# Kernel optimization log

Measured on AMD Instinct MI355X. Metric: run time of the kernel, lower is better.

## Reference

```python
import jax, jax.numpy as jnp
import numpy as np

B, V, L = 2, 12000, 16
IN_F = 479  # 3+3+3+9+3+10+64+256(imgf)+128(gar_latent)


def setup_inputs() -> dict:
    key = jax.random.key(0)
    ks = jax.random.split(key, 12)

    def w(k, shape, fan_in):
        return (jax.random.normal(k, shape, jnp.float32) / np.sqrt(fan_in)).astype(jnp.float32)

    return {
        "x": jax.random.normal(ks[0], (B, V, IN_F), jnp.float32),
        "spiral_idx": jax.random.randint(ks[1], (V + 1, L), 0, V + 1),  # indices incl. dummy vertex V
        "W_point": w(ks[2], (IN_F, 256), IN_F),                 # pointMLP Linear, no bias
        "res1_W": w(ks[3], (2, 256 * L, 256), 256 * L),          # two SpiralConv(256,256)
        "res1_b": jnp.zeros((2, 256), jnp.float32),
        "W_mid": w(ks[4], (256, 128), 256),                      # midDown, no bias
        "ress_W": w(ks[5], (3, 2, 128 * L, 128), 128 * L),       # 3 residual blocks of SpiralConv(128,128)
        "ress_b": jnp.zeros((3, 2, 128), jnp.float32),
        "Wo1": w(ks[6], (512, 256), 512), "bo1": jnp.zeros((256,), jnp.float32),
        "Wo2": w(ks[7], (256, 128), 256), "bo2": jnp.zeros((128,), jnp.float32),
        "Wo3": w(ks[8], (128, 3), 128),  "bo3": jnp.zeros((3,), jnp.float32),
    }


def _spiral_conv(x, idx, Wc, bc, zp):
    # x: [B, Vp, C]; idx: [Vp, L] -> gather spiral neighborhoods then linear, mask dummy vertex
    Bn, Vp, C = x.shape
    g = x[:, idx.reshape(-1), :].reshape(Bn, Vp, -1)  # [B, Vp, L*C]
    return (g @ Wc + bc) * zp


def _res_block(x, idx, Wb, bb, zp):
    h = jax.nn.relu(_spiral_conv(x, idx, Wb[0], bb[0], zp))
    h = _spiral_conv(h, idx, Wb[1], bb[1], zp)
    return jax.nn.relu(h + x)


def reference(x, spiral_idx, W_point, res1_W, res1_b, W_mid, ress_W, ress_b,
              Wo1, bo1, Wo2, bo2, Wo3, bo3):
    pf = jax.nn.relu(x @ W_point)                                  # [B, V, 256]
    Bn = pf.shape[0]
    pfs = jnp.concatenate([pf, jnp.zeros((Bn, 1, pf.shape[-1]), pf.dtype)], axis=1)  # [B, V+1, 256]
    Vp = pfs.shape[1]
    zp = jnp.ones((1, Vp, 1), pf.dtype).at[0, -1, 0].set(0.0)       # zero_padding mask
    fs = (_res_block(pfs, spiral_idx, res1_W, res1_b, zp) @ W_mid) * zp  # [B, Vp, 128]
    gfs = jnp.max(fs[:, :-1, :], axis=1, keepdims=True)             # masked global max-pool [B,1,128]
    for i in range(3):
        fs = _res_block(fs, spiral_idx, ress_W[i], ress_b[i], zp)
    g = jnp.broadcast_to(gfs, (Bn, Vp, gfs.shape[-1])) * zp
    h = jnp.concatenate([pfs, fs, g], axis=-1)                      # [B, Vp, 512]
    h = jax.nn.relu(h @ Wo1 + bo1)
    h = jax.nn.relu(h @ Wo2 + bo2)
    out = h @ Wo3 + bo3
    return out[:, :-1, :]                                           # drop dummy vertex
```

## Files before the change

kernel.cpp:

```cpp
#include <hip/hip_runtime.h>
#include <cstdint>
#include <cfloat>
#include <cstddef>

constexpr int BATCH  = 2;
constexpr int V      = 12000;
constexpr int VP     = V + 1;
constexpr int M_ROWS = BATCH * VP;
constexpr int L_SP   = 16;

typedef _Float16 half_t;
typedef _Float16 half8 __attribute__((ext_vector_type(8)));
typedef float floatx4 __attribute__((ext_vector_type(4)));

__device__ __forceinline__ void async_cp16(const void* g, void* l) {
    __builtin_amdgcn_global_load_lds(
        (const __attribute__((address_space(1))) unsigned int*)g,
        (__attribute__((address_space(3))) unsigned int*)l, 16, 0, 0);
}

template<bool GATHER, int BM>
__global__ __launch_bounds__(256, 2)
void gemm_mfma(const half_t* __restrict__ A, const half_t* __restrict__ Wt,
               const float* __restrict__ bias, const half_t* __restrict__ res,
               const int* __restrict__ idx, half_t* __restrict__ out,
               int M, int N, int K, int lgC, int KA, int relu, int mask)
{
    constexpr int AF = BM / 32;
    __shared__ half_t As[BM * 32];
    __shared__ half_t Bs[128 * 32];

    const int tid  = threadIdx.x;
    const int lane = tid & 63;
    const int w    = tid >> 6;
    const int bm   = blockIdx.x, bn = blockIdx.y;

    const int sb = (((tid & 3) ^ ((tid >> 3) & 3)) << 3);

    const int brow = tid >> 2;
    const half_t* w0 = Wt + (size_t)(bn * 128 + brow) * K + sb;
    const half_t* w1 = Wt + (size_t)(bn * 128 + 64 + brow) * K + sb;
    half_t* lB0 = &Bs[(size_t)tid * 8];
    half_t* lB1 = &Bs[(size_t)(tid + 256) * 8];

    const bool astage = (BM == 64) ? true : (tid < 128);
    const int arow = tid >> 2;
    int m0 = bm * BM + arow; if (m0 >= M) m0 = M - 1;
    const int b0 = m0 / VP, v0 = m0 - b0 * VP;
    const half_t* a0 = GATHER ? nullptr : (A + (size_t)m0 * KA + sb);
    half_t* lA0 = &As[(size_t)tid * 8];

    const int wm = (w >> 1) * (BM / 2);
    const int wn = (w & 1) << 6;
    const int fr = lane & 15;
    const int qs = (((lane >> 4) ^ ((fr >> 1) & 3)) << 3);

    floatx4 acc[AF][4] = {};

    int curl = -1;
    const half_t* g0 = nullptr;
    const int Cm1 = (1 << lgC) - 1;

    const int nk = K >> 5;
    for (int t = 0; t < nk; ++t) {
        const int k0 = t << 5;
        if (astage) {
            if (GATHER) {
                const int l = k0 >> lgC;
                if (l != curl) {
                    curl = l;
                    const int j0 = idx[(v0 << 4) + l];
                    g0 = A + (((size_t)(b0 * VP + j0)) << lgC) + sb;
                }
                async_cp16(g0 + (k0 & Cm1), lA0);
            } else {
                async_cp16(a0 + k0, lA0);
            }
        }
        async_cp16(w0 + k0, lB0);
        async_cp16(w1 + k0, lB1);
        __syncthreads();

        half8 af[AF], bf[4];
#pragma unroll
        for (int i = 0; i < AF; ++i)
            af[i] = *(const half8*)&As[(wm + (i << 4) + fr) * 32 + qs];
#pragma unroll
        for (int j = 0; j < 4; ++j)
            bf[j] = *(const half8*)&Bs[(wn + (j << 4) + fr) * 32 + qs];
#pragma unroll
        for (int i = 0; i < AF; ++i)
#pragma unroll
            for (int j = 0; j < 4; ++j)
                acc[i][j] = __builtin_amdgcn_mfma_f32_16x16x32_f16(af[i], bf[j], acc[i][j], 0, 0, 0);
        __syncthreads();
    }

    const int er = (lane >> 4) << 2;
#pragma unroll
    for (int i = 0; i < AF; ++i) {
#pragma unroll
        for (int j = 0; j < 4; ++j) {
            const int n = bn * 128 + wn + (j << 4) + fr;
            const floatx4 a = acc[i][j];
#pragma unroll
            for (int r = 0; r < 4; ++r) {
                const int m = bm * BM + wm + (i << 4) + er + r;
                if (m >= M) continue;
                float val = a[r];
                if (bias) val += bias[n];
                if (res)  val += (float)res[(size_t)m * N + n];
                if (relu) val = fmaxf(val, 0.f);
                const int vv = m - (m / VP) * VP;
                if (mask && vv == VP - 1) val = 0.f;
                out[(size_t)m * N + n] = (half_t)val;
            }
        }
    }
}

__global__ void wcvt(const float* __restrict__ in, half_t* __restrict__ out,
                     int K, int N, int Kpad)
{
    __shared__ float t[32][33];
    const size_t ioff = (size_t)blockIdx.z * K * N;
    const size_t ooff = (size_t)blockIdx.z * N * Kpad;
    const int k0 = blockIdx.x * 32, n0 = blockIdx.y * 32;
    const int tx = threadIdx.x & 31, ty = threadIdx.x >> 5;
#pragma unroll
    for (int r = 0; r < 4; ++r) {
        const int k = k0 + ty + r * 8;
        t[ty + r * 8][tx] = (k < K && n0 + tx < N) ? in[ioff + (size_t)k * N + n0 + tx] : 0.f;
    }
    __syncthreads();
#pragma unroll
    for (int r = 0; r < 4; ++r) {
        const int n = n0 + ty + r * 8;
        const int k = k0 + tx;
        if (n < N && k < Kpad) out[ooff + (size_t)n * Kpad + k] = (half_t)t[tx][ty + r * 8];
    }
}

__global__ void cvt_x(const float* __restrict__ x, half_t* __restrict__ xh)
{
    const int m = blockIdx.x;
    const int b = m / VP, v = m - b * VP;
    for (int k = threadIdx.x; k < 480; k += 256) {
        float val = (v < V && k < 479) ? x[((size_t)b * V + v) * 479 + k] : 0.f;
        xh[(size_t)m * 480 + k] = (half_t)val;
    }
}

__global__ void maxpool1(const half_t* __restrict__ fs, float* __restrict__ pmax)
{
    const int b = blockIdx.x, chunk = blockIdx.y;
    const int c = threadIdx.x;
    const int v0 = chunk * (V / 32);
    float m = -FLT_MAX;
    const half_t* p = fs + ((size_t)b * VP + v0) * 128 + c;
    for (int v = 0; v < V / 32; ++v) { m = fmaxf(m, (float)*p); p += 128; }
    pmax[((size_t)b * 32 + chunk) * 128 + c] = m;
}
__global__ void maxpool2(const float* __restrict__ pmax, half_t* __restrict__ gfs)
{
    const int b = blockIdx.x, c = threadIdx.x;
    float m = -FLT_MAX;
    for (int i = 0; i < 32; ++i) m = fmaxf(m, pmax[((size_t)b * 32 + i) * 128 + c]);
    gfs[b * 128 + c] = (half_t)m;
}

__global__ void concat_k(const half_t* __restrict__ pfs, const half_t* __restrict__ fs,
                         const half_t* __restrict__ gfs, half_t* __restrict__ h)
{
    const size_t i = (size_t)blockIdx.x * 256 + threadIdx.x;
    if (i >= (size_t)M_ROWS * 512) return;
    const int    n   = (int)(i & 511);
    const size_t row = i >> 9;
    const int    b   = (int)(row / VP);
    const int    v   = (int)(row - (size_t)b * VP);
    half_t val;
    if (n < 256)      val = pfs[row * 256 + n];
    else if (n < 384) val = fs[row * 128 + (n - 256)];
    else              val = (v == VP - 1) ? (half_t)0.f : gfs[b * 128 + (n - 384)];
    h[i] = val;
}

__global__ void final_k(const half_t* __restrict__ h, const float* __restrict__ Wo3,
                        const float* __restrict__ bo3, float* __restrict__ out)
{
    __shared__ float wsm[384];
    __shared__ float b3[3];
    for (int t = threadIdx.x; t < 384; t += 256) wsm[t] = Wo3[t];
    if (threadIdx.x < 3) b3[threadIdx.x] = bo3[threadIdx.x];
    __syncthreads();

    const int gid = blockIdx.x * 256 + threadIdx.x;
    if (gid >= BATCH * V) return;
    const int b = gid / V;
    const int v = gid - b * V;
    const half_t* hr = h + ((size_t)b * VP + v) * 128;

    float o0 = b3[0], o1 = b3[1], o2 = b3[2];
#pragma unroll 4
    for (int c = 0; c < 128; ++c) {
        const float hv = (float)hr[c];
        o0 += hv * wsm[c * 3 + 0];
        o1 += hv * wsm[c * 3 + 1];
        o2 += hv * wsm[c * 3 + 2];
    }
    out[(size_t)gid * 3 + 0] = o0;
    out[(size_t)gid * 3 + 1] = o1;
    out[(size_t)gid * 3 + 2] = o2;
}

extern "C" void kernel_launch(void* const* d_in, const int* in_sizes, int n_in,
                              void* d_out, int out_size, void* d_ws, size_t ws_size,
                              hipStream_t stream)
{
    const float* x       = (const float*)d_in[0];
    const int*   sidx    = (const int*)  d_in[1];
    const float* W_point = (const float*)d_in[2];
    const float* res1_W  = (const float*)d_in[3];
    const float* res1_b  = (const float*)d_in[4];
    const float* W_mid   = (const float*)d_in[5];
    const float* ress_W  = (const float*)d_in[6];
    const float* ress_b  = (const float*)d_in[7];
    const float* Wo1     = (const float*)d_in[8];
    const float* bo1     = (const float*)d_in[9];
    const float* Wo2     = (const float*)d_in[10];
    const float* bo2     = (const float*)d_in[11];
    const float* Wo3     = (const float*)d_in[12];
    const float* bo3     = (const float*)d_in[13];
    float* out = (float*)d_out;

    char* p = (char*)d_ws;
    auto alloc = [&](size_t bytes) { char* q = p; p += (bytes + 255) & ~(size_t)255; return q; };
    const size_t fs_bytes = (size_t)M_ROWS * 128 * 2;
    half_t* reg0 = (half_t*)alloc((size_t)M_ROWS * 512 * 2);
    half_t* pfs  = (half_t*)alloc((size_t)M_ROWS * 256 * 2);
    char*   rA   = alloc((size_t)M_ROWS * 256 * 2);
    char*   rB   = alloc((size_t)M_ROWS * 256 * 2);
    half_t* Wpt_t  = (half_t*)alloc((size_t)256 * 480 * 2);
    half_t* r1Wt   = (half_t*)alloc((size_t)2 * 256 * 4096 * 2);
    half_t* Wmid_t = (half_t*)alloc((size_t)128 * 256 * 2);
    half_t* rsWt   = (half_t*)alloc((size_t)6 * 128 * 2048 * 2);
    half_t* Wo1_t  = (half_t*)alloc((size_t)256 * 512 * 2);
    half_t* Wo2_t  = (half_t*)alloc((size_t)128 * 256 * 2);
    float*  pmax   = (float*)alloc((size_t)2 * 32 * 128 * 4);
    half_t* gfs    = (half_t*)alloc(512);

    half_t* bufA = (half_t*)rA;
    half_t* bufB = (half_t*)rB;
    half_t* fsA  = (half_t*)rA;
    half_t* fsB  = (half_t*)(rA + fs_bytes);
    half_t* tmp  = (half_t*)rB;
    half_t* h512 = reg0;
    half_t* h256 = (half_t*)rB;
    half_t* h128 = (half_t*)rA;

    const dim3 blk(256);

    wcvt<<<dim3(15, 8, 1),  blk, 0, stream>>>(W_point, Wpt_t, 479, 256, 480);
    wcvt<<<dim3(128, 8, 2), blk, 0, stream>>>(res1_W, r1Wt, 4096, 256, 4096);
    wcvt<<<dim3(8, 4, 1),   blk, 0, stream>>>(W_mid, Wmid_t, 256, 128, 256);
    wcvt<<<dim3(64, 4, 6),  blk, 0, stream>>>(ress_W, rsWt, 2048, 128, 2048);
    wcvt<<<dim3(16, 8, 1),  blk, 0, stream>>>(Wo1, Wo1_t, 512, 256, 512);
    wcvt<<<dim3(8, 4, 1),   blk, 0, stream>>>(Wo2, Wo2_t, 256, 128, 256);
    cvt_x<<<M_ROWS, blk, 0, stream>>>(x, reg0);

    const int mg64 = (M_ROWS + 63) / 64;
    const int mg32 = (M_ROWS + 31) / 32;

    gemm_mfma<false, 64><<<dim3(mg64, 2), blk, 0, stream>>>(
        reg0, Wpt_t, nullptr, nullptr, nullptr, pfs,
        M_ROWS, 256, 480, 0, 480, 1, 1);

    gemm_mfma<true, 64><<<dim3(mg64, 2), blk, 0, stream>>>(
        pfs, r1Wt, res1_b, nullptr, sidx, bufA,
        M_ROWS, 256, 4096, 8, 0, 1, 1);

    gemm_mfma<true, 64><<<dim3(mg64, 2), blk, 0, stream>>>(
        bufA, r1Wt + (size_t)256 * 4096, res1_b + 256, pfs, sidx, bufB,
        M_ROWS, 256, 4096, 8, 0, 1, 1);

    gemm_mfma<false, 32><<<dim3(mg32, 1), blk, 0, stream>>>(
        bufB, Wmid_t, nullptr, nullptr, nullptr, fsA,
        M_ROWS, 128, 256, 0, 256, 0, 1);

    maxpool1<<<dim3(BATCH, 32), dim3(128), 0, stream>>>(fsA, pmax);
    maxpool2<<<dim3(BATCH), dim3(128), 0, stream>>>(pmax, gfs);

    half_t* cur = fsA;
    half_t* nxt = fsB;
    for (int i = 0; i < 3; ++i) {
        const half_t* Wa = rsWt + (size_t)(2 * i + 0) * 128 * 2048;
        const half_t* Wb = rsWt + (size_t)(2 * i + 1) * 128 * 2048;
        const float* ba = ress_b + (2 * i + 0) * 128;
        const float* bb = ress_b + (2 * i + 1) * 128;
        gemm_mfma<true, 32><<<dim3(mg32, 1), blk, 0, stream>>>(
            cur, Wa, ba, nullptr, sidx, tmp,
            M_ROWS, 128, 2048, 7, 0, 1, 1);
        gemm_mfma<true, 32><<<dim3(mg32, 1), blk, 0, stream>>>(
            tmp, Wb, bb, cur, sidx, nxt,
            M_ROWS, 128, 2048, 7, 0, 1, 1);
        half_t* t2 = cur; cur = nxt; nxt = t2;
    }

    concat_k<<<(unsigned)(((size_t)M_ROWS * 512 + 255) / 256), blk, 0, stream>>>(
        pfs, cur, gfs, h512);

    gemm_mfma<false, 64><<<dim3(mg64, 2), blk, 0, stream>>>(
        h512, Wo1_t, bo1, nullptr, nullptr, h256,
        M_ROWS, 256, 512, 0, 512, 1, 0);

    gemm_mfma<false, 32><<<dim3(mg32, 1), blk, 0, stream>>>(
        h256, Wo2_t, bo2, nullptr, nullptr, h128,
        M_ROWS, 128, 256, 0, 256, 1, 0);

    final_k<<<(BATCH * V + 255) / 256, blk, 0, stream>>>(h128, Wo3, bo3, out);
}
```

Baseline: 678.3 us.

## Retile GEMM to BN=64, BK=64 with 8-way swizzle and higher occupancy

The MFMA GEMM now uses N tiles of 64 instead of 128 and K steps of 64 instead of 32, with a new XOR swizzle over 8 chunks and two MFMA sub-steps per iteration. The grid doubles in the N dimension and launch bounds move to 4 waves per SIMD, so more blocks run per CU and there are half as many barriers per K. The channel shift becomes a template parameter, and the x input and point weights are padded to K=512 so it divides by 64. In exchange, the gathered A rows are fetched once per N tile, so the number of A gathers doubles.

```diff
diff --git a/kernel.cpp b/kernel.cpp
--- a/kernel.cpp
+++ b/kernel.cpp
@@ -19,89 +19,105 @@
         (__attribute__((address_space(3))) unsigned int*)l, 16, 0, 0);
 }
 
-template<bool GATHER, int BM>
-__global__ __launch_bounds__(256, 2)
+template<bool GATHER, int BM, int LGC>
+__global__ __launch_bounds__(256, 4)
 void gemm_mfma(const half_t* __restrict__ A, const half_t* __restrict__ Wt,
                const float* __restrict__ bias, const half_t* __restrict__ res,
                const int* __restrict__ idx, half_t* __restrict__ out,
-               int M, int N, int K, int lgC, int KA, int relu, int mask)
+               int M, int N, int K, int KA, int relu, int mask)
 {
     constexpr int AF = BM / 32;
-    __shared__ half_t As[BM * 32];
-    __shared__ half_t Bs[128 * 32];
+    __shared__ half_t As[BM * 64];
+    __shared__ half_t Bs[64 * 64];
 
     const int tid  = threadIdx.x;
     const int lane = tid & 63;
     const int w    = tid >> 6;
     const int bm   = blockIdx.x, bn = blockIdx.y;
 
-    const int sb = (((tid & 3) ^ ((tid >> 3) & 3)) << 3);
-
-    const int brow = tid >> 2;
-    const half_t* w0 = Wt + (size_t)(bn * 128 + brow) * K + sb;
-    const half_t* w1 = Wt + (size_t)(bn * 128 + 64 + brow) * K + sb;
-    half_t* lB0 = &Bs[(size_t)tid * 8];
-    half_t* lB1 = &Bs[(size_t)(tid + 256) * 8];
-
-    const bool astage = (BM == 64) ? true : (tid < 128);
-    const int arow = tid >> 2;
-    int m0 = bm * BM + arow; if (m0 >= M) m0 = M - 1;
-    const int b0 = m0 / VP, v0 = m0 - b0 * VP;
-    const half_t* a0 = GATHER ? nullptr : (A + (size_t)m0 * KA + sb);
-    half_t* lA0 = &As[(size_t)tid * 8];
+    const int goff = (((lane & 7) ^ ((lane >> 3) & 7)) << 3);
+    const int rsub = lane >> 3;
+
+    const int nB0 = bn * 64 + (w << 3) + rsub;
+    const half_t* wp0 = Wt + (size_t)nB0 * K + goff;
+    const half_t* wp1 = Wt + (size_t)(nB0 + 32) * K + goff;
+    half_t* lB0 = &Bs[(size_t)((w << 6) + lane) * 8];
+    half_t* lB1 = &Bs[(size_t)(((w + 4) << 6) + lane) * 8];
+
+    int bb[AF], vv[AF];
+    const half_t* aP[AF];
+    half_t* lA[AF];
+#pragma unroll
+    for (int ai = 0; ai < AF; ++ai) {
+        const int blk = w + (ai << 2);
+        int m = bm * BM + (blk << 3) + rsub;
+        if (m >= M) m = M - 1;
+        bb[ai] = m / VP; vv[ai] = m - bb[ai] * VP;
+        aP[ai] = GATHER ? nullptr : (A + (size_t)m * KA + goff);
+        lA[ai] = &As[(size_t)((blk << 6) + lane) * 8];
+    }
 
     const int wm = (w >> 1) * (BM / 2);
-    const int wn = (w & 1) << 6;
+    const int wn = (w & 1) << 5;
     const int fr = lane & 15;
-    const int qs = (((lane >> 4) ^ ((fr >> 1) & 3)) << 3);
-
-    floatx4 acc[AF][4] = {};
+    const int q  = lane >> 4;
+    const int f7 = fr & 7;
+
+    floatx4 acc[AF][2] = {};
 
     int curl = -1;
-    const half_t* g0 = nullptr;
-    const int Cm1 = (1 << lgC) - 1;
-
-    const int nk = K >> 5;
+    const half_t* gp[AF];
+    const int Cm1 = (1 << LGC) - 1;
+
+    const int nk = K >> 6;
     for (int t = 0; t < nk; ++t) {
-        const int k0 = t << 5;
-        if (astage) {
-            if (GATHER) {
-                const int l = k0 >> lgC;
-                if (l != curl) {
-                    curl = l;
-                    const int j0 = idx[(v0 << 4) + l];
-                    g0 = A + (((size_t)(b0 * VP + j0)) << lgC) + sb;
+        const int k0 = t << 6;
+        if (GATHER) {
+            const int l = k0 >> LGC;
+            if (l != curl) {
+                curl = l;
+#pragma unroll
+                for (int ai = 0; ai < AF; ++ai) {
+                    const int j = idx[(vv[ai] << 4) + l];
+                    gp[ai] = A + (((size_t)(bb[ai] * VP + j)) << LGC) + goff;
                 }
-                async_cp16(g0 + (k0 & Cm1), lA0);
-            } else {
-                async_cp16(a0 + k0, lA0);
             }
+            const int ko = k0 & Cm1;
+#pragma unroll
+            for (int ai = 0; ai < AF; ++ai) async_cp16(gp[ai] + ko, lA[ai]);
+        } else {
+#pragma unroll
+            for (int ai = 0; ai < AF; ++ai) async_cp16(aP[ai] + k0, lA[ai]);
         }
-        async_cp16(w0 + k0, lB0);
-        async_cp16(w1 + k0, lB1);
+        async_cp16(wp0 + k0, lB0);
+        async_cp16(wp1 + k0, lB1);
         __syncthreads();
 
-        half8 af[AF], bf[4];
-#pragma unroll
-        for (int i = 0; i < AF; ++i)
-            af[i] = *(const half8*)&As[(wm + (i << 4) + fr) * 32 + qs];
-#pragma unroll
-        for (int j = 0; j < 4; ++j)
-            bf[j] = *(const half8*)&Bs[(wn + (j << 4) + fr) * 32 + qs];
-#pragma unroll
-        for (int i = 0; i < AF; ++i)
-#pragma unroll
-            for (int j = 0; j < 4; ++j)
-                acc[i][j] = __builtin_amdgcn_mfma_f32_16x16x32_f16(af[i], bf[j], acc[i][j], 0, 0, 0);
+#pragma unroll
+        for (int s = 0; s < 2; ++s) {
+            const int ck = ((((s << 2) | q) ^ f7) << 3);
+            half8 af[AF], bf[2];
+#pragma unroll
+            for (int i = 0; i < AF; ++i)
+                af[i] = *(const half8*)&As[(wm + (i << 4) + fr) * 64 + ck];
+#pragma unroll
+            for (int j = 0; j < 2; ++j)
+                bf[j] = *(const half8*)&Bs[(wn + (j << 4) + fr) * 64 + ck];
+#pragma unroll
+            for (int i = 0; i < AF; ++i)
+#pragma unroll
+                for (int j = 0; j < 2; ++j)
+                    acc[i][j] = __builtin_amdgcn_mfma_f32_16x16x32_f16(af[i], bf[j], acc[i][j], 0, 0, 0);
+        }
         __syncthreads();
     }
 
-    const int er = (lane >> 4) << 2;
+    const int er = q << 2;
 #pragma unroll
     for (int i = 0; i < AF; ++i) {
 #pragma unroll
-        for (int j = 0; j < 4; ++j) {
-            const int n = bn * 128 + wn + (j << 4) + fr;
+        for (int j = 0; j < 2; ++j) {
+            const int n = bn * 64 + wn + (j << 4) + fr;
             const floatx4 a = acc[i][j];
 #pragma unroll
             for (int r = 0; r < 4; ++r) {
@@ -111,8 +127,8 @@
                 if (bias) val += bias[n];
                 if (res)  val += (float)res[(size_t)m * N + n];
                 if (relu) val = fmaxf(val, 0.f);
-                const int vv = m - (m / VP) * VP;
-                if (mask && vv == VP - 1) val = 0.f;
+                const int vvm = m - (m / VP) * VP;
+                if (mask && vvm == VP - 1) val = 0.f;
                 out[(size_t)m * N + n] = (half_t)val;
             }
         }
@@ -145,9 +161,9 @@
 {
     const int m = blockIdx.x;
     const int b = m / VP, v = m - b * VP;
-    for (int k = threadIdx.x; k < 480; k += 256) {
+    for (int k = threadIdx.x; k < 512; k += 256) {
         float val = (v < V && k < 479) ? x[((size_t)b * V + v) * 479 + k] : 0.f;
-        xh[(size_t)m * 480 + k] = (half_t)val;
+        xh[(size_t)m * 512 + k] = (half_t)val;
     }
 }
 
@@ -240,7 +256,7 @@
     half_t* pfs  = (half_t*)alloc((size_t)M_ROWS * 256 * 2);
     char*   rA   = alloc((size_t)M_ROWS * 256 * 2);
     char*   rB   = alloc((size_t)M_ROWS * 256 * 2);
-    half_t* Wpt_t  = (half_t*)alloc((size_t)256 * 480 * 2);
+    half_t* Wpt_t  = (half_t*)alloc((size_t)256 * 512 * 2);
     half_t* r1Wt   = (half_t*)alloc((size_t)2 * 256 * 4096 * 2);
     half_t* Wmid_t = (half_t*)alloc((size_t)128 * 256 * 2);
     half_t* rsWt   = (half_t*)alloc((size_t)6 * 128 * 2048 * 2);
@@ -260,7 +276,7 @@
 
     const dim3 blk(256);
 
-    wcvt<<<dim3(15, 8, 1),  blk, 0, stream>>>(W_point, Wpt_t, 479, 256, 480);
+    wcvt<<<dim3(16, 8, 1),  blk, 0, stream>>>(W_point, Wpt_t, 479, 256, 512);
     wcvt<<<dim3(128, 8, 2), blk, 0, stream>>>(res1_W, r1Wt, 4096, 256, 4096);
     wcvt<<<dim3(8, 4, 1),   blk, 0, stream>>>(W_mid, Wmid_t, 256, 128, 256);
     wcvt<<<dim3(64, 4, 6),  blk, 0, stream>>>(ress_W, rsWt, 2048, 128, 2048);
@@ -271,21 +287,21 @@
     const int mg64 = (M_ROWS + 63) / 64;
     const int mg32 = (M_ROWS + 31) / 32;
 
-    gemm_mfma<false, 64><<<dim3(mg64, 2), blk, 0, stream>>>(
+    gemm_mfma<false, 64, 0><<<dim3(mg64, 4), blk, 0, stream>>>(
         reg0, Wpt_t, nullptr, nullptr, nullptr, pfs,
-        M_ROWS, 256, 480, 0, 480, 1, 1);
-
-    gemm_mfma<true, 64><<<dim3(mg64, 2), blk, 0, stream>>>(
+        M_ROWS, 256, 512, 512, 1, 1);
+
+    gemm_mfma<true, 64, 8><<<dim3(mg64, 4), blk, 0, stream>>>(
         pfs, r1Wt, res1_b, nullptr, sidx, bufA,
-        M_ROWS, 256, 4096, 8, 0, 1, 1);
-
-    gemm_mfma<true, 64><<<dim3(mg64, 2), blk, 0, stream>>>(
+        M_ROWS, 256, 4096, 0, 1, 1);
+
+    gemm_mfma<true, 64, 8><<<dim3(mg64, 4), blk, 0, stream>>>(
         bufA, r1Wt + (size_t)256 * 4096, res1_b + 256, pfs, sidx, bufB,
-        M_ROWS, 256, 4096, 8, 0, 1, 1);
-
-    gemm_mfma<false, 32><<<dim3(mg32, 1), blk, 0, stream>>>(
+        M_ROWS, 256, 4096, 0, 1, 1);
+
+    gemm_mfma<false, 32, 0><<<dim3(mg32, 2), blk, 0, stream>>>(
         bufB, Wmid_t, nullptr, nullptr, nullptr, fsA,
-        M_ROWS, 128, 256, 0, 256, 0, 1);
+        M_ROWS, 128, 256, 256, 0, 1);
 
     maxpool1<<<dim3(BATCH, 32), dim3(128), 0, stream>>>(fsA, pmax);
     maxpool2<<<dim3(BATCH), dim3(128), 0, stream>>>(pmax, gfs);
@@ -297,25 +313,25 @@
         const half_t* Wb = rsWt + (size_t)(2 * i + 1) * 128 * 2048;
         const float* ba = ress_b + (2 * i + 0) * 128;
         const float* bb = ress_b + (2 * i + 1) * 128;
-        gemm_mfma<true, 32><<<dim3(mg32, 1), blk, 0, stream>>>(
+        gemm_mfma<true, 32, 7><<<dim3(mg32, 2), blk, 0, stream>>>(
             cur, Wa, ba, nullptr, sidx, tmp,
-            M_ROWS, 128, 2048, 7, 0, 1, 1);
-        gemm_mfma<true, 32><<<dim3(mg32, 1), blk, 0, stream>>>(
+            M_ROWS, 128, 2048, 0, 1, 1);
+        gemm_mfma<true, 32, 7><<<dim3(mg32, 2), blk, 0, stream>>>(
             tmp, Wb, bb, cur, sidx, nxt,
-            M_ROWS, 128, 2048, 7, 0, 1, 1);
+            M_ROWS, 128, 2048, 0, 1, 1);
         half_t* t2 = cur; cur = nxt; nxt = t2;
     }
 
     concat_k<<<(unsigned)(((size_t)M_ROWS * 512 + 255) / 256), blk, 0, stream>>>(
         pfs, cur, gfs, h512);
 
-    gemm_mfma<false, 64><<<dim3(mg64, 2), blk, 0, stream>>>(
+    gemm_mfma<false, 64, 0><<<dim3(mg64, 4), blk, 0, stream>>>(
         h512, Wo1_t, bo1, nullptr, nullptr, h256,
-        M_ROWS, 256, 512, 0, 512, 1, 0);
-
-    gemm_mfma<false, 32><<<dim3(mg32, 1), blk, 0, stream>>>(
+        M_ROWS, 256, 512, 512, 1, 0);
+
+    gemm_mfma<false, 32, 0><<<dim3(mg32, 2), blk, 0, stream>>>(
         h256, Wo2_t, bo2, nullptr, nullptr, h128,
-        M_ROWS, 128, 256, 0, 256, 1, 0);
+        M_ROWS, 128, 256, 256, 1, 0);
 
     final_k<<<(BATCH * V + 255) / 256, blk, 0, stream>>>(h128, Wo3, bo3, out);
 }
```

New measurement: 638.5 us. 1.06x faster.
